# Kernel optimization log

Measured on AMD Instinct MI355X. Metric: run time of the kernel, lower is better.

The kernel has to match this reference:

```python
import jax, jax.numpy as jnp
import numpy as np

XBAR = 128            # XBAR_ROW_SIZE == XBAR_COL_SIZE (PUMA crossbar)
WB, WF = 16, 12       # weight_bits, weight_bit_frac
IB, IF = 16, 12       # input_bits, input_bit_frac
BIT_SLICE, NSLICE = 2, 8      # weight_bits // bit_slice slices per weight
BIT_STREAM, NSTREAM = 1, 16   # input_bits // bit_stream streams
ADC_BIT = 9           # log2(128) + bit_slice
ACM_BITS, ACM_FRAC = 16, 12
STRIDE, PAD, K = 1, 1, 3


def setup_inputs() -> dict:
    key = jax.random.key(0)
    k1, k2 = jax.random.split(key)
    x = jax.random.normal(k1, (4, 64, 16, 16), jnp.float32)
    # modest weight scale so the 16-bit accumulator (range ~ +/-8) is not saturated
    w = 0.05 * jax.random.normal(k2, (128, 64, 3, 3), jnp.float32)
    return {"x": x, "w": w}


def _extract_patches(xpad, k, stride):
    # xpad: [B, C, Hp, Wp] -> [B, OH*OW, C*k*k] with (c, ki, kj) channel order (== torch unfold)
    B, C, Hp, Wp = xpad.shape
    OH = (Hp - k) // stride + 1
    OW = (Wp - k) // stride + 1
    cols = []
    for ki in range(k):
        for kj in range(k):
            cols.append(xpad[:, :, ki:ki + OH * stride:stride, kj:kj + OW * stride:stride])
    p = jnp.stack(cols, axis=2)                      # [B, C, k*k, OH, OW]
    return p.reshape(B, C * k * k, OH * OW).transpose(0, 2, 1), OH, OW


def _bit_slice_weights(w_mag):
    # w_mag [Cout, L] nonneg -> padded crossbar matrix [Lp, Cout*NSLICE], MSB slice first
    Cout, L = w_mag.shape
    w_int = jnp.clip(jnp.round(w_mag * (1 << WF)), 0, (1 << WB) - 1).astype(jnp.int32)
    shifts = (BIT_SLICE * jnp.arange(NSLICE - 1, -1, -1)).astype(jnp.int32)
    slices = (w_int[..., None] >> shifts) & ((1 << BIT_SLICE) - 1)   # [Cout, L, NSLICE]
    mat = slices.transpose(1, 0, 2).reshape(L, Cout * NSLICE).astype(jnp.float32)
    Lp = -(-L // XBAR) * XBAR
    return jnp.pad(mat, ((0, Lp - L), (0, 0)))


def _mvm(bits, Wm):
    # bits [P, R, XBAR, T] binary streams; Wm [R, XBAR, J] conductance slices.
    # Per-crossbar analog column sums -> ADC quantize -> shift-add slices & streams.
    analog = jnp.einsum('prkt,rkj->prjt', bits, Wm)
    adc = jnp.clip(jnp.round(analog), 0.0, float((1 << ADC_BIT) - 1))
    P, R, J, T = adc.shape
    adc = adc.reshape(P, R, J // NSLICE, NSLICE, T)
    sl_w = (2.0 ** (BIT_SLICE * jnp.arange(NSLICE - 1, -1, -1))).astype(jnp.float32)
    st_w = (2.0 ** jnp.arange(NSTREAM)).astype(jnp.float32)
    st_w = st_w.at[-1].multiply(-1.0)   # two's-complement sign bit (bit_stream == 1 path)
    return jnp.einsum('prcst,s,t->pc', adc, sl_w, st_w)   # sums over crossbar rows too


def mvm_conv(x, w):
    B, Cin, H, W = x.shape
    Cout = w.shape[0]
    xpad = jnp.pad(x, ((0, 0), (0, 0), (PAD, PAD), (PAD, PAD)))
    patches, OH, OW = _extract_patches(xpad, K, STRIDE)
    L = Cin * K * K
    P = B * OH * OW
    v = patches.reshape(P, L)
    # input fixed point -> 16-bit two's complement bit streams, LSB first
    x_int = jnp.round(v * (1 << IF)).astype(jnp.int32)
    x_u = x_int & ((1 << IB) - 1)
    bits = ((x_u[..., None] >> jnp.arange(IB, dtype=jnp.int32)) & 1).astype(jnp.float32)
    Lp = -(-L // XBAR) * XBAR
    bits = jnp.pad(bits, ((0, 0), (0, Lp - L), (0, 0))).reshape(P, Lp // XBAR, XBAR, NSTREAM)
    wf = w.reshape(Cout, L)
    Wpos = _bit_slice_weights(jnp.clip(wf, 0.0, None)).reshape(Lp // XBAR, XBAR, Cout * NSLICE)
    Wneg = _bit_slice_weights(jnp.abs(jnp.clip(wf, None, 0.0))).reshape(Lp // XBAR, XBAR, Cout * NSLICE)
    out = (_mvm(bits, Wpos) - _mvm(bits, Wneg)) / float(1 << (WF + IF))
    # accumulator fixed-point quantization (acm_bits / acm_bit_frac)
    scale = float(1 << ACM_FRAC)
    lo, hi = float(-(1 << (ACM_BITS - 1))), float((1 << (ACM_BITS - 1)) - 1)
    out = jnp.clip(jnp.round(out * scale), lo, hi) / scale
    return out.reshape(B, OH, OW, Cout).transpose(0, 3, 1, 2)


def reference(x, w):
    return mvm_conv(x, w)
```

## Files before the change

### kernel.cpp

```cpp
#include <hip/hip_runtime.h>


#define CIN 64
#define COUT 128
#define HW 16
#define LDIM 576
#define LP (LDIM / 2)
#define NPIX 1024
#define QS 4096.0f

typedef short short2v __attribute__((ext_vector_type(2)));

__device__ inline int dot2(int a, int b, int c) {
#if __has_builtin(__builtin_amdgcn_sdot2)
    union { int i; short2v v; } ua, ub;
    ua.i = a; ub.i = b;
    return __builtin_amdgcn_sdot2(ua.v, ub.v, c, false);
#else
    return c + (int)(short)(a & 0xFFFF) * (int)(short)(b & 0xFFFF)
             + (a >> 16) * (b >> 16);
#endif
}

__global__ __launch_bounds__(256) void prep_kernel(const float* __restrict__ x,
                                                   const float* __restrict__ w,
                                                   int* __restrict__ wq2,
                                                   int* __restrict__ xq2) {
    int tid = blockIdx.x * 256 + threadIdx.x;
    if (tid < NPIX * LP) {
        int p = tid / LP, lp = tid - p * LP;
        int b = p >> 8, oh = (p >> 4) & 15, ow = p & 15;
        int s[2];
#pragma unroll
        for (int j = 0; j < 2; ++j) {
            int l = lp * 2 + j;
            int cin = l / 9, r = l - cin * 9, ki = r / 3, kj = r - ki * 3;
            int ih = oh - 1 + ki, iw = ow - 1 + kj;
            float v = 0.0f;
            if ((unsigned)ih < HW && (unsigned)iw < HW)
                v = x[((b * CIN + cin) * HW + ih) * HW + iw];
            s[j] = (int)rintf(v * QS);
        }
        xq2[tid] = (int)(((unsigned)(unsigned short)(short)s[1] << 16) |
                         (unsigned short)(short)s[0]);
    } else {
        int j = tid - NPIX * LP;
        if (j < COUT * LP) {
            int c = j / LP, lp = j - c * LP;
            int s0 = (int)rintf(w[c * LDIM + lp * 2 + 0] * QS);
            int s1 = (int)rintf(w[c * LDIM + lp * 2 + 1] * QS);
            wq2[lp * COUT + c] = (int)(((unsigned)(unsigned short)(short)s1 << 16) |
                                       (unsigned short)(short)s0);
        }
    }
}

__global__ __launch_bounds__(256) void conv_kernel(const int* __restrict__ xq2,
                                                   const int* __restrict__ wq2,
                                                   float* __restrict__ out) {
    __shared__ int4 xs[4][LP / 4];
    const int tid = threadIdx.x;
    const int p0 = blockIdx.x * 4;
    const int b = p0 >> 8, oh = (p0 >> 4) & 15, ow0 = p0 & 15;

    const int4* src = (const int4*)(xq2 + p0 * LP);
    for (int i = tid; i < 4 * LP / 4; i += 256)
        ((int4*)xs)[i] = src[i];
    __syncthreads();

    const int c = tid & 127, h = tid >> 7;
    const int4* xA = xs[2 * h];
    const int4* xB = xs[2 * h + 1];
    int acc0 = 0, acc1 = 0;
#pragma unroll 8
    for (int q = 0; q < LP / 4; ++q) {
        int4 xa = xA[q], xb = xB[q];
        int w0 = wq2[(q * 4 + 0) * COUT + c];
        int w1 = wq2[(q * 4 + 1) * COUT + c];
        int w2 = wq2[(q * 4 + 2) * COUT + c];
        int w3 = wq2[(q * 4 + 3) * COUT + c];
        acc0 = dot2(xa.x, w0, dot2(xa.y, w1, dot2(xa.z, w2, dot2(xa.w, w3, acc0))));
        acc1 = dot2(xb.x, w0, dot2(xb.y, w1, dot2(xb.z, w2, dot2(xb.w, w3, acc1))));
    }

    int accs[2] = {acc0, acc1};
#pragma unroll
    for (int j = 0; j < 2; ++j) {
        int a = accs[j];
        int f = a >> 12, r = a & 4095;
        int q = f + ((r > 2048) || (r == 2048 && (f & 1)));
        q = min(max(q, -32768), 32767);
        int ow = ow0 + 2 * h + j;
        out[((b * COUT + c) * HW + oh) * HW + ow] = (float)q * (1.0f / QS);
    }
}

extern "C" void kernel_launch(void* const* d_in, const int* in_sizes, int n_in,
                              void* d_out, int out_size, void* d_ws, size_t ws_size,
                              hipStream_t stream) {
    const float* x = (const float*)d_in[0];
    const float* w = (const float*)d_in[1];
    float* out = (float*)d_out;
    int* wq2 = (int*)d_ws;
    int* xq2 = (int*)((char*)d_ws + LP * COUT * sizeof(int));

    int prep_jobs = NPIX * LP + COUT * LP;
    prep_kernel<<<prep_jobs / 256, 256, 0, stream>>>(x, w, wq2, xq2);
    conv_kernel<<<NPIX / 4, 256, 0, stream>>>(xq2, wq2, out);
}
```

Baseline: 63.27 us.

## Fuse quantization prep into conv kernel with channel-tiled shared-memory weights

Merges the separate prep kernel into the conv kernel. Each block quantizes and packs a 32-output-channel slice of weights into shared memory and builds a 16-pixel row of packed input patches in shared memory, then runs the dot2 loop. This removes a kernel launch and the global workspace round trip. In exchange, each block redundantly re-quantizes the weights and im2col data that were previously computed once, and shared memory use grows to about 55 KB per block.

New measurement: 68.13 us. 1.08x slower.

```diff
diff --git a/kernel.cpp b/kernel.cpp
--- a/kernel.cpp
+++ b/kernel.cpp
@@ -5,9 +5,10 @@
 #define COUT 128
 #define HW 16
 #define LDIM 576
-#define LP (LDIM / 2)
-#define NPIX 1024
+#define LP 288
 #define QS 4096.0f
+#define CC 32
+#define PXT 16
 
 typedef short short2v __attribute__((ext_vector_type(2)));
 
@@ -22,77 +23,88 @@
 #endif
 }
 
-__global__ __launch_bounds__(256) void prep_kernel(const float* __restrict__ x,
-                                                   const float* __restrict__ w,
-                                                   int* __restrict__ wq2,
-                                                   int* __restrict__ xq2) {
-    int tid = blockIdx.x * 256 + threadIdx.x;
-    if (tid < NPIX * LP) {
-        int p = tid / LP, lp = tid - p * LP;
-        int b = p >> 8, oh = (p >> 4) & 15, ow = p & 15;
-        int s[2];
-#pragma unroll
-        for (int j = 0; j < 2; ++j) {
-            int l = lp * 2 + j;
-            int cin = l / 9, r = l - cin * 9, ki = r / 3, kj = r - ki * 3;
-            int ih = oh - 1 + ki, iw = ow - 1 + kj;
-            float v = 0.0f;
-            if ((unsigned)ih < HW && (unsigned)iw < HW)
-                v = x[((b * CIN + cin) * HW + ih) * HW + iw];
-            s[j] = (int)rintf(v * QS);
-        }
-        xq2[tid] = (int)(((unsigned)(unsigned short)(short)s[1] << 16) |
-                         (unsigned short)(short)s[0]);
-    } else {
-        int j = tid - NPIX * LP;
-        if (j < COUT * LP) {
-            int c = j / LP, lp = j - c * LP;
-            int s0 = (int)rintf(w[c * LDIM + lp * 2 + 0] * QS);
-            int s1 = (int)rintf(w[c * LDIM + lp * 2 + 1] * QS);
-            wq2[lp * COUT + c] = (int)(((unsigned)(unsigned short)(short)s1 << 16) |
-                                       (unsigned short)(short)s0);
+__device__ inline int pack16(int s0, int s1) {
+    return (int)(((unsigned)(unsigned short)(short)s1 << 16) |
+                 (unsigned short)(short)s0);
+}
+
+__global__ __launch_bounds__(256) void fused_conv_kernel(const float* __restrict__ x,
+                                                         const float* __restrict__ w,
+                                                         float* __restrict__ out) {
+    __shared__ int ws2[144 * 64];
+    __shared__ int xs[PXT][LP];
+
+    const int tid = threadIdx.x;
+    const int ctile = blockIdx.x & 3;
+    const int pxtile = blockIdx.x >> 2;
+    const int c0 = ctile * CC;
+    const int b  = pxtile >> 4;
+    const int oh = pxtile & 15;
+
+    {
+        const int cc = tid & 31, kb = tid >> 5;
+        const float4* w4 = (const float4*)w;
+        #pragma unroll
+        for (int k = 0; k < 18; ++k) {
+            int lp2 = kb + k * 8;
+            float4 wv = w4[(c0 + cc) * 144 + lp2];
+            int i0 = (int)rintf(wv.x * QS);
+            int i1 = (int)rintf(wv.y * QS);
+            int i2 = (int)rintf(wv.z * QS);
+            int i3 = (int)rintf(wv.w * QS);
+            ((int2*)ws2)[lp2 * 32 + cc] = make_int2(pack16(i0, i1), pack16(i2, i3));
         }
     }
-}
 
-__global__ __launch_bounds__(256) void conv_kernel(const int* __restrict__ xq2,
-                                                   const int* __restrict__ wq2,
-                                                   float* __restrict__ out) {
-    __shared__ int4 xs[4][LP / 4];
-    const int tid = threadIdx.x;
-    const int p0 = blockIdx.x * 4;
-    const int b = p0 >> 8, oh = (p0 >> 4) & 15, ow0 = p0 & 15;
-
-    const int4* src = (const int4*)(xq2 + p0 * LP);
-    for (int i = tid; i < 4 * LP / 4; i += 256)
-        ((int4*)xs)[i] = src[i];
+    {
+        const int px = tid >> 4;
+        const int j  = tid & 15;
+        #pragma unroll 2
+        for (int t = 0; t < 18; ++t) {
+            int lp = j * 18 + t;
+            int s[2];
+            #pragma unroll
+            for (int u = 0; u < 2; ++u) {
+                int l = lp * 2 + u;
+                int cin = l / 9, r = l - cin * 9, ki = r / 3, kj = r - ki * 3;
+                int ih = oh - 1 + ki, iw = px - 1 + kj;
+                float v = 0.0f;
+                if ((unsigned)ih < HW && (unsigned)iw < HW)
+                    v = x[((b * CIN + cin) * HW + ih) * HW + iw];
+                s[u] = (int)rintf(v * QS);
+            }
+            xs[px][lp] = pack16(s[0], s[1]);
+        }
+    }
     __syncthreads();
 
-    const int c = tid & 127, h = tid >> 7;
-    const int4* xA = xs[2 * h];
-    const int4* xB = xs[2 * h + 1];
+    const int c  = tid & 31;
+    const int pp = tid >> 5;
+    const int4* xA = (const int4*)xs[2 * pp];
+    const int4* xB = (const int4*)xs[2 * pp + 1];
+    const int2* wp = (const int2*)ws2;
     int acc0 = 0, acc1 = 0;
-#pragma unroll 8
-    for (int q = 0; q < LP / 4; ++q) {
+    #pragma unroll 8
+    for (int q = 0; q < 72; ++q) {
         int4 xa = xA[q], xb = xB[q];
-        int w0 = wq2[(q * 4 + 0) * COUT + c];
-        int w1 = wq2[(q * 4 + 1) * COUT + c];
-        int w2 = wq2[(q * 4 + 2) * COUT + c];
-        int w3 = wq2[(q * 4 + 3) * COUT + c];
-        acc0 = dot2(xa.x, w0, dot2(xa.y, w1, dot2(xa.z, w2, dot2(xa.w, w3, acc0))));
-        acc1 = dot2(xb.x, w0, dot2(xb.y, w1, dot2(xb.z, w2, dot2(xb.w, w3, acc1))));
+        int2 wA = wp[(2 * q) * 32 + c];
+        int2 wB = wp[(2 * q + 1) * 32 + c];
+        acc0 = dot2(xa.x, wA.x, dot2(xa.y, wA.y, dot2(xa.z, wB.x, dot2(xa.w, wB.y, acc0))));
+        acc1 = dot2(xb.x, wA.x, dot2(xb.y, wA.y, dot2(xb.z, wB.x, dot2(xb.w, wB.y, acc1))));
     }
 
     int accs[2] = {acc0, acc1};
-#pragma unroll
-    for (int j = 0; j < 2; ++j) {
-        int a = accs[j];
+    float o[2];
+    #pragma unroll
+    for (int jj = 0; jj < 2; ++jj) {
+        int a = accs[jj];
         int f = a >> 12, r = a & 4095;
         int q = f + ((r > 2048) || (r == 2048 && (f & 1)));
         q = min(max(q, -32768), 32767);
-        int ow = ow0 + 2 * h + j;
-        out[((b * COUT + c) * HW + oh) * HW + ow] = (float)q * (1.0f / QS);
+        o[jj] = (float)q * (1.0f / QS);
     }
+    float2* o2 = (float2*)&out[(((b * COUT + c0 + c) * HW + oh) * HW) + 2 * pp];
+    *o2 = make_float2(o[0], o[1]);
 }
 
 extern "C" void kernel_launch(void* const* d_in, const int* in_sizes, int n_in,
@@ -101,10 +113,5 @@
     const float* x = (const float*)d_in[0];
     const float* w = (const float*)d_in[1];
     float* out = (float*)d_out;
-    int* wq2 = (int*)d_ws;
-    int* xq2 = (int*)((char*)d_ws + LP * COUT * sizeof(int));
-
-    int prep_jobs = NPIX * LP + COUT * LP;
-    prep_kernel<<<prep_jobs / 256, 256, 0, stream>>>(x, w, wq2, xq2);
-    conv_kernel<<<NPIX / 4, 256, 0, stream>>>(xq2, wq2, out);
+    fused_conv_kernel<<<256, 256, 0, stream>>>(x, w, out);
 }
```
